# Performance work log

Hardware: AMD Instinct MI355X
Metric: run time of the kernel (lower is better)

## Reference

```python
import jax, jax.numpy as jnp
import numpy as np

T, H, E, I = 512, 2048, 8, 4096
W_SCALE = 0.02  # keep activations numerically sane with randn weights


def setup_inputs() -> dict:
    key = jax.random.key(0)
    k_x, k_r, k_w1, k_w3, k_w2 = jax.random.split(key, 5)
    x = jax.random.normal(k_x, (T, H), dtype=jnp.float32)
    router_logits = jax.random.normal(k_r, (T, E), dtype=jnp.float32)
    w1 = jax.random.normal(k_w1, (E, I, H), dtype=jnp.float32) * W_SCALE  # gate proj (silu branch)
    w3 = jax.random.normal(k_w3, (E, I, H), dtype=jnp.float32) * W_SCALE  # up proj
    w2 = jax.random.normal(k_w2, (E, H, I), dtype=jnp.float32) * W_SCALE  # down proj
    return {"x": x, "router_logits": router_logits, "w1": w1, "w3": w3, "w2": w2}


def reference(x, router_logits, w1, w3, w2):
    # Llama4 routing: top-1 expert, router weight = sigmoid(top logit),
    # applied on the INPUT (apply_router_weight_on_input=True).
    top_logit = jnp.max(router_logits, axis=-1)          # [T]
    expert_idx = jnp.argmax(router_logits, axis=-1)      # [T] int
    scale = jax.nn.sigmoid(top_logit)                    # [T]
    xs = x * scale[:, None]                              # [T, H]

    # Grouped SwiGLU experts (dense over E, combined with one-hot select;
    # faithful to fused grouped-GEMM math of FusedMoE).
    gate = jnp.einsum('th,eih->eti', xs, w1)             # [E, T, I]
    up = jnp.einsum('th,eih->eti', xs, w3)               # [E, T, I]
    h = jax.nn.silu(gate) * up                           # [E, T, I]
    y = jnp.einsum('eti,ehi->eth', h, w2)                # [E, T, H]

    onehot = jax.nn.one_hot(expert_idx, E, dtype=x.dtype)  # [T, E]
    out = jnp.einsum('te,eth->th', onehot, y)            # [T, H]
    return out
```

## Files before the change

kernel.cpp:

```cpp
#include <hip/hip_runtime.h>

#define T_TOK 512
#define HDIM 2048
#define NEXP 8
#define IDIM 4096

typedef float f32x4 __attribute__((ext_vector_type(4)));
typedef __bf16 bf16x8 __attribute__((ext_vector_type(8)));
typedef unsigned short ushort8 __attribute__((ext_vector_type(8)));

static __device__ __forceinline__ unsigned short f2bf(float f) {
    unsigned int u = __float_as_uint(f);
    u = (u + 0x7fffu + ((u >> 16) & 1u)) >> 16;
    return (unsigned short)u;
}

static __device__ __forceinline__ bf16x8 cvt8(const f32x4 lo, const f32x4 hi) {
    bf16x8 r;
#pragma unroll
    for (int q = 0; q < 4; ++q) { r[q] = (__bf16)lo[q]; r[q + 4] = (__bf16)hi[q]; }
    return r;
}

static __device__ __forceinline__ void gload_lds16(const void* g, void* l) {
    auto gp = reinterpret_cast<const unsigned int __attribute__((address_space(1)))*>(
        reinterpret_cast<unsigned long long>(g));
    auto lp = reinterpret_cast<unsigned int __attribute__((address_space(3)))*>(
        static_cast<unsigned int>(reinterpret_cast<unsigned long long>(l)));
    __builtin_amdgcn_global_load_lds(gp, lp, 16, 0, 0);
}

static __device__ __forceinline__ void gload_lds16_nt(const void* g, void* l) {
    auto gp = reinterpret_cast<const unsigned int __attribute__((address_space(1)))*>(
        reinterpret_cast<unsigned long long>(g));
    auto lp = reinterpret_cast<unsigned int __attribute__((address_space(3)))*>(
        static_cast<unsigned int>(reinterpret_cast<unsigned long long>(l)));
    __builtin_amdgcn_global_load_lds(gp, lp, 16, 0, 2 );
}

__global__ void k_route(const float* __restrict__ logits,
                        int* __restrict__ off, int* __restrict__ tok,
                        float* __restrict__ scale) {
    __shared__ int cnt[NEXP], cur[NEXP];
    const int t = threadIdx.x;
    if (t < NEXP) cnt[t] = 0;
    __syncthreads();
    float m = logits[t * NEXP];
    int a = 0;
#pragma unroll
    for (int j = 1; j < NEXP; ++j) {
        float v = logits[t * NEXP + j];
        if (v > m) { m = v; a = j; }
    }
    scale[t] = 1.f / (1.f + __expf(-m));
    atomicAdd(&cnt[a], 1);
    __syncthreads();
    if (t == 0) {
        int o = 0;
        for (int e = 0; e < NEXP; ++e) { off[e] = o; cur[e] = o; o += cnt[e]; }
        off[NEXP] = o;
    }
    __syncthreads();
    int r = atomicAdd(&cur[a], 1);
    tok[r] = t;
}

__global__ void k_gather(const float* __restrict__ x, const int* __restrict__ tok,
                         const float* __restrict__ scale,
                         unsigned short* __restrict__ xs) {
    const int pos = blockIdx.x;
    const int t = tok[pos];
    const float s = scale[t];
    const int c = threadIdx.x * 8;
    const float4* src = (const float4*)(x + (size_t)t * HDIM + c);
    float4 v0 = src[0], v1 = src[1];
    ushort8 o;
    o[0] = f2bf(v0.x * s); o[1] = f2bf(v0.y * s);
    o[2] = f2bf(v0.z * s); o[3] = f2bf(v0.w * s);
    o[4] = f2bf(v1.x * s); o[5] = f2bf(v1.y * s);
    o[6] = f2bf(v1.z * s); o[7] = f2bf(v1.w * s);
    *(ushort8*)(xs + (size_t)pos * HDIM + c) = o;
}

__global__ void __launch_bounds__(512, 4)
k_moe1(const unsigned short* __restrict__ xs,
       const float* __restrict__ w1,
       const float* __restrict__ w3,
       const int* __restrict__ off,
       unsigned short* __restrict__ hbuf) {
    __shared__ char smem[49152];

    const int tid = threadIdx.x;
    const int w = tid >> 6, l = tid & 63;
    const int wr = w >> 2, wc = w & 3;
    const int e = blockIdx.x & 7;
    const int n0 = (blockIdx.x >> 3) * 64;
    const int ks0 = (blockIdx.x * 13) & 31;
    const int pos_beg = off[e], pos_end = off[e + 1];

    const char* w1b = (const char*)(w1 + (size_t)e * IDIM * HDIM);
    const char* w3b = (const char*)(w3 + (size_t)e * IDIM * HDIM);
    const char* xsb = (const char*)xs;

    const int ia = w * 2;
    const int arow_off = l >> 3;
    const int asw = ((l & 7) ^ (l >> 3)) << 4;
    const int brow_off = l >> 4;

    for (int m0 = pos_beg; m0 < pos_end; m0 += 128) {
        f32x4 accG[4], accU[4];
#pragma unroll
        for (int i = 0; i < 4; ++i) { accG[i] = (f32x4){0,0,0,0}; accU[i] = (f32x4){0,0,0,0}; }

#pragma unroll 1
        for (int it = 0; it < HDIM / 64; ++it) {
            const int ks = (it + ks0) & 31;
            const int k0 = ks * 64;
#pragma unroll
            for (int j = 0; j < 2; ++j) {
                const int i = ia + j;
                int gr = m0 + i * 8 + arow_off; if (gr > T_TOK - 1) gr = T_TOK - 1;
                gload_lds16(xsb + (size_t)gr * (HDIM * 2) + k0 * 2 + asw, smem + i * 1024);
            }
#pragma unroll
            for (int j = 0; j < 2; ++j) {
                const int i = ia + j;
                const int r = i * 4 + brow_off;
                const size_t so = (size_t)(n0 + r) * (HDIM * 4) + k0 * 4 +
                                  (((l & 15) << 4) ^ ((r & 7) << 4));
                gload_lds16_nt(w1b + so, smem + 16384 + i * 1024);
                gload_lds16_nt(w3b + so, smem + 32768 + i * 1024);
            }
            __syncthreads();

#pragma unroll
            for (int kk = 0; kk < 2; ++kk) {
                bf16x8 a[4];
#pragma unroll
                for (int fm = 0; fm < 4; ++fm) {
                    const int row = wr * 64 + fm * 16 + (l & 15);
                    const int kb = (kk * 64 + ((l >> 4) << 4)) ^ ((l & 7) << 4);
                    a[fm] = *(const bf16x8*)(smem + row * 128 + kb);
                }
                const int rB = wc * 16 + (l & 15);
                const int p0 = (kk * 128 + ((l >> 4) << 5)) ^ ((l & 7) << 4);
                const char* pg = smem + 16384 + rB * 256;
                const char* pu = smem + 32768 + rB * 256;
                f32x4 g0 = *(const f32x4*)(pg + p0);
                f32x4 g1 = *(const f32x4*)(pg + (p0 ^ 16));
                f32x4 u0 = *(const f32x4*)(pu + p0);
                f32x4 u1 = *(const f32x4*)(pu + (p0 ^ 16));
                bf16x8 bg = cvt8(g0, g1);
                bf16x8 bu = cvt8(u0, u1);
#pragma unroll
                for (int fm = 0; fm < 4; ++fm) {
                    accG[fm] = __builtin_amdgcn_mfma_f32_16x16x32_bf16(
                        a[fm], bg, accG[fm], 0, 0, 0);
                    accU[fm] = __builtin_amdgcn_mfma_f32_16x16x32_bf16(
                        a[fm], bu, accU[fm], 0, 0, 0);
                }
            }
            __syncthreads();
        }

#pragma unroll
        for (int fm = 0; fm < 4; ++fm)
#pragma unroll
            for (int r = 0; r < 4; ++r) {
                const int pos = m0 + wr * 64 + fm * 16 + (l >> 4) * 4 + r;
                if (pos < pos_end) {
                    const float gv = accG[fm][r];
                    const float uv = accU[fm][r];
                    const float hv = gv / (1.f + __expf(-gv)) * uv;
                    hbuf[(size_t)pos * IDIM + n0 + wc * 16 + (l & 15)] = f2bf(hv);
                }
            }
    }
}

__global__ void __launch_bounds__(256, 4)
k_moe2(const unsigned short* __restrict__ hbuf,
       const float* __restrict__ w2,
       const int* __restrict__ off,
       const int* __restrict__ tok,
       float* __restrict__ out) {
    __shared__ char smem[20480];

    const int tid = threadIdx.x;
    const int w = tid >> 6, l = tid & 63;
    const int e = blockIdx.x & 7;
    const int n0 = (blockIdx.x >> 3) * 16;
    const int ks0 = (blockIdx.x * 13) & 63;
    const int pos_beg = off[e], pos_end = off[e + 1];
    const char* w2b = (const char*)(w2 + (size_t)e * HDIM * IDIM);
    const char* hb  = (const char*)hbuf;

    const int ia = w * 4;
    const int arow_off = l >> 3;
    const int asw = ((l & 7) ^ (l >> 3)) << 4;
    const int brow_off = l >> 4;

    for (int m0 = pos_beg; m0 < pos_end; m0 += 128) {
        f32x4 acc[2];
        acc[0] = (f32x4){0,0,0,0}; acc[1] = (f32x4){0,0,0,0};

#pragma unroll 1
        for (int it = 0; it < IDIM / 64; ++it) {
            const int ks = (it + ks0) & 63;
            const int k0 = ks * 64;
#pragma unroll
            for (int j = 0; j < 4; ++j) {
                const int i = ia + j;
                int gr = m0 + i * 8 + arow_off; if (gr > T_TOK - 1) gr = T_TOK - 1;
                gload_lds16(hb + (size_t)gr * (IDIM * 2) + k0 * 2 + asw, smem + i * 1024);
            }
            {
                const int r = w * 4 + brow_off;
                const size_t so = (size_t)(n0 + r) * (IDIM * 4) + k0 * 4 +
                                  (((l & 15) << 4) ^ ((r & 7) << 4));
                gload_lds16(w2b + so, smem + 16384 + w * 1024);
            }
            __syncthreads();

#pragma unroll
            for (int kk = 0; kk < 2; ++kk) {
                const int rB = l & 15;
                const int p0 = (kk * 128 + ((l >> 4) << 5)) ^ ((l & 7) << 4);
                const char* pb = smem + 16384 + rB * 256;
                f32x4 b0 = *(const f32x4*)(pb + p0);
                f32x4 b1 = *(const f32x4*)(pb + (p0 ^ 16));
                bf16x8 bb = cvt8(b0, b1);
#pragma unroll
                for (int fm = 0; fm < 2; ++fm) {
                    const int row = w * 32 + fm * 16 + (l & 15);
                    const int kb = (kk * 64 + ((l >> 4) << 4)) ^ ((l & 7) << 4);
                    bf16x8 a = *(const bf16x8*)(smem + row * 128 + kb);
                    acc[fm] = __builtin_amdgcn_mfma_f32_16x16x32_bf16(a, bb, acc[fm], 0, 0, 0);
                }
            }
            __syncthreads();
        }

#pragma unroll
        for (int fm = 0; fm < 2; ++fm)
#pragma unroll
            for (int r = 0; r < 4; ++r) {
                const int pos = m0 + w * 32 + fm * 16 + (l >> 4) * 4 + r;
                if (pos < pos_end) {
                    const int t = tok[pos];
                    out[(size_t)t * HDIM + n0 + (l & 15)] = acc[fm][r];
                }
            }
    }
}

extern "C" void kernel_launch(void* const* d_in, const int* in_sizes, int n_in,
                              void* d_out, int out_size, void* d_ws, size_t ws_size,
                              hipStream_t stream) {
    const float* x      = (const float*)d_in[0];
    const float* logits = (const float*)d_in[1];
    const float* w1     = (const float*)d_in[2];
    const float* w3     = (const float*)d_in[3];
    const float* w2     = (const float*)d_in[4];
    float* out = (float*)d_out;

    char* ws = (char*)d_ws;
    int* off   = (int*)ws;
    int* tok   = (int*)(ws + 64);
    float* scl = (float*)(ws + 64 + 2048);
    unsigned short* xs   = (unsigned short*)(ws + 8192);
    unsigned short* hbuf = (unsigned short*)(ws + 8192 + (size_t)T_TOK * HDIM * 2);

    k_route<<<1, T_TOK, 0, stream>>>(logits, off, tok, scl);
    k_gather<<<T_TOK, 256, 0, stream>>>(x, tok, scl, xs);
    k_moe1<<<NEXP * (IDIM / 64), 512, 0, stream>>>(xs, w1, w3, off, hbuf);
    k_moe2<<<NEXP * (HDIM / 16), 256, 0, stream>>>(hbuf, w2, off, tok, out);
}
```

Measured before the change: 185.0 us.

## Restructure gate/up GEMM to stage weight rows whole in LDS and read activations from global

```diff
diff --git a/kernel.cpp b/kernel.cpp
--- a/kernel.cpp
+++ b/kernel.cpp
@@ -82,98 +82,87 @@
     *(ushort8*)(xs + (size_t)pos * HDIM + c) = o;
 }
 
-__global__ void __launch_bounds__(512, 4)
+__global__ void __launch_bounds__(256, 2)
 k_moe1(const unsigned short* __restrict__ xs,
        const float* __restrict__ w1,
        const float* __restrict__ w3,
        const int* __restrict__ off,
        unsigned short* __restrict__ hbuf) {
-    __shared__ char smem[49152];
+    __shared__ char smem[65536];
 
     const int tid = threadIdx.x;
     const int w = tid >> 6, l = tid & 63;
-    const int wr = w >> 2, wc = w & 3;
     const int e = blockIdx.x & 7;
-    const int n0 = (blockIdx.x >> 3) * 64;
-    const int ks0 = (blockIdx.x * 13) & 31;
+    const int n0 = (blockIdx.x >> 3) * 8;
     const int pos_beg = off[e], pos_end = off[e + 1];
 
     const char* w1b = (const char*)(w1 + (size_t)e * IDIM * HDIM);
     const char* w3b = (const char*)(w3 + (size_t)e * IDIM * HDIM);
-    const char* xsb = (const char*)xs;
-
-    const int ia = w * 2;
-    const int arow_off = l >> 3;
-    const int asw = ((l & 7) ^ (l >> 3)) << 4;
-    const int brow_off = l >> 4;
 
     for (int m0 = pos_beg; m0 < pos_end; m0 += 128) {
-        f32x4 accG[4], accU[4];
-#pragma unroll
-        for (int i = 0; i < 4; ++i) { accG[i] = (f32x4){0,0,0,0}; accU[i] = (f32x4){0,0,0,0}; }
+        const unsigned short* pA[2];
+#pragma unroll
+        for (int fm = 0; fm < 2; ++fm) {
+            int gr = m0 + w * 32 + fm * 16 + (l & 15);
+            if (gr > T_TOK - 1) gr = T_TOK - 1;
+            pA[fm] = xs + (size_t)gr * HDIM + (l >> 4) * 8;
+        }
+
+        f32x4 acc[2];
+        acc[0] = (f32x4){0, 0, 0, 0};
+        acc[1] = (f32x4){0, 0, 0, 0};
 
 #pragma unroll 1
-        for (int it = 0; it < HDIM / 64; ++it) {
-            const int ks = (it + ks0) & 31;
-            const int k0 = ks * 64;
-#pragma unroll
-            for (int j = 0; j < 2; ++j) {
-                const int i = ia + j;
-                int gr = m0 + i * 8 + arow_off; if (gr > T_TOK - 1) gr = T_TOK - 1;
-                gload_lds16(xsb + (size_t)gr * (HDIM * 2) + k0 * 2 + asw, smem + i * 1024);
-            }
-#pragma unroll
-            for (int j = 0; j < 2; ++j) {
-                const int i = ia + j;
-                const int r = i * 4 + brow_off;
-                const size_t so = (size_t)(n0 + r) * (HDIM * 4) + k0 * 4 +
-                                  (((l & 15) << 4) ^ ((r & 7) << 4));
-                gload_lds16_nt(w1b + so, smem + 16384 + i * 1024);
-                gload_lds16_nt(w3b + so, smem + 32768 + i * 1024);
-            }
-            __syncthreads();
-
-#pragma unroll
-            for (int kk = 0; kk < 2; ++kk) {
-                bf16x8 a[4];
-#pragma unroll
-                for (int fm = 0; fm < 4; ++fm) {
-                    const int row = wr * 64 + fm * 16 + (l & 15);
-                    const int kb = (kk * 64 + ((l >> 4) << 4)) ^ ((l & 7) << 4);
-                    a[fm] = *(const bf16x8*)(smem + row * 128 + kb);
-                }
-                const int rB = wc * 16 + (l & 15);
-                const int p0 = (kk * 128 + ((l >> 4) << 5)) ^ ((l & 7) << 4);
-                const char* pg = smem + 16384 + rB * 256;
-                const char* pu = smem + 32768 + rB * 256;
-                f32x4 g0 = *(const f32x4*)(pg + p0);
-                f32x4 g1 = *(const f32x4*)(pg + (p0 ^ 16));
-                f32x4 u0 = *(const f32x4*)(pu + p0);
-                f32x4 u1 = *(const f32x4*)(pu + (p0 ^ 16));
-                bf16x8 bg = cvt8(g0, g1);
-                bf16x8 bu = cvt8(u0, u1);
-#pragma unroll
-                for (int fm = 0; fm < 4; ++fm) {
-                    accG[fm] = __builtin_amdgcn_mfma_f32_16x16x32_bf16(
-                        a[fm], bg, accG[fm], 0, 0, 0);
-                    accU[fm] = __builtin_amdgcn_mfma_f32_16x16x32_bf16(
-                        a[fm], bu, accU[fm], 0, 0, 0);
+        for (int ko = 0; ko < 2; ++ko) {
+#pragma unroll
+            for (int j = 0; j < 4; ++j) {
+                const int ridx = w * 4 + j;
+                const int s = ridx & 7;
+                const char* rb = (ridx < 8)
+                    ? w1b + (size_t)(n0 + ridx) * (HDIM * 4)
+                    : w3b + (size_t)(n0 + ridx - 8) * (HDIM * 4);
+                const int lg = (l & 56) | ((l & 7) ^ s);
+#pragma unroll
+                for (int c = 0; c < 4; ++c) {
+                    gload_lds16_nt(rb + ko * 4096 + ((c * 64 + lg) << 4),
+                                   smem + ridx * 4096 + c * 1024);
+                }
+            }
+            asm volatile("s_waitcnt vmcnt(0)" ::: "memory");
+            __syncthreads();
+
+            const int ridx = l & 15;
+            const int s = ridx & 7;
+            const char* sb = smem + ridx * 4096;
+#pragma unroll 4
+            for (int kk = 0; kk < 32; ++kk) {
+                const int g0 = kk * 8 + (l >> 4) * 2;
+                const int g1 = g0 + 1;
+                f32x4 b0 = *(const f32x4*)(sb + (((g0 & ~7) | ((g0 & 7) ^ s)) << 4));
+                f32x4 b1 = *(const f32x4*)(sb + (((g1 & ~7) | ((g1 & 7) ^ s)) << 4));
+                bf16x8 bb = cvt8(b0, b1);
+#pragma unroll
+                for (int fm = 0; fm < 2; ++fm) {
+                    bf16x8 a = *(const bf16x8*)(pA[fm] + ko * 1024 + kk * 32);
+                    acc[fm] = __builtin_amdgcn_mfma_f32_16x16x32_bf16(
+                        a, bb, acc[fm], 0, 0, 0);
                 }
             }
             __syncthreads();
         }
 
 #pragma unroll
-        for (int fm = 0; fm < 4; ++fm)
+        for (int fm = 0; fm < 2; ++fm)
 #pragma unroll
             for (int r = 0; r < 4; ++r) {
-                const int pos = m0 + wr * 64 + fm * 16 + (l >> 4) * 4 + r;
-                if (pos < pos_end) {
-                    const float gv = accG[fm][r];
-                    const float uv = accU[fm][r];
-                    const float hv = gv / (1.f + __expf(-gv)) * uv;
-                    hbuf[(size_t)pos * IDIM + n0 + wc * 16 + (l & 15)] = f2bf(hv);
-                }
+                const float own = acc[fm][r];
+                const float oth = __shfl_xor(own, 8);
+                const float gate = (l & 8) ? oth : own;
+                const float up   = (l & 8) ? own : oth;
+                const float hv = gate / (1.f + __expf(-gate)) * up;
+                const int pos = m0 + w * 32 + fm * 16 + (l >> 4) * 4 + r;
+                if (!(l & 8) && pos < pos_end)
+                    hbuf[(size_t)pos * IDIM + n0 + (l & 7)] = f2bf(hv);
             }
     }
 }
@@ -202,7 +191,8 @@
 
     for (int m0 = pos_beg; m0 < pos_end; m0 += 128) {
         f32x4 acc[2];
-        acc[0] = (f32x4){0,0,0,0}; acc[1] = (f32x4){0,0,0,0};
+        acc[0] = (f32x4){0, 0, 0, 0};
+        acc[1] = (f32x4){0, 0, 0, 0};
 
 #pragma unroll 1
         for (int it = 0; it < IDIM / 64; ++it) {
@@ -273,6 +263,6 @@
 
     k_route<<<1, T_TOK, 0, stream>>>(logits, off, tok, scl);
     k_gather<<<T_TOK, 256, 0, stream>>>(x, tok, scl, xs);
-    k_moe1<<<NEXP * (IDIM / 64), 512, 0, stream>>>(xs, w1, w3, off, hbuf);
+    k_moe1<<<NEXP * (IDIM / 8), 256, 0, stream>>>(xs, w1, w3, off, hbuf);
     k_moe2<<<NEXP * (HDIM / 16), 256, 0, stream>>>(hbuf, w2, off, tok, out);
 }
```

New measurement: 360.5 us. 94.8% more time.
